# Performance work log

Hardware: AMD Instinct MI355X
Metric: run time of the kernel (lower is better)

The kernel has to match this reference:

```python
import jax, jax.numpy as jnp
import numpy as np
from jax import lax

D_MODEL = 1024
D_STATE = 16
D_CONV = 4
EXPAND = 2
D_INNER = D_MODEL * EXPAND
EPS = 1e-6


def setup_inputs() -> dict:
    key = jax.random.key(0)
    ks = jax.random.split(key, 8)
    B, L = 2, 1024
    x = jax.random.normal(ks[0], (B, L, D_MODEL), dtype=jnp.float32)
    norm_w = jnp.ones((D_MODEL,), jnp.float32)
    W_in = jax.random.normal(ks[1], (2 * D_INNER, D_MODEL), jnp.float32) * (1.0 / np.sqrt(D_MODEL))
    conv_w = jax.random.normal(ks[2], (D_INNER, 1, D_CONV), jnp.float32) * (1.0 / np.sqrt(D_CONV))
    conv_b = jnp.zeros((D_INNER,), jnp.float32)
    W_x = jax.random.normal(ks[3], (2 * D_STATE + 1, D_INNER), jnp.float32) * (1.0 / np.sqrt(D_INNER))
    A_log = jnp.log(jnp.broadcast_to(jnp.arange(1, D_STATE + 1, dtype=jnp.float32), (D_INNER, D_STATE)))
    D_skip = jnp.ones((D_INNER,), jnp.float32)
    W_dt = jax.random.normal(ks[4], (D_INNER, 1), jnp.float32)
    b_dt = jax.random.normal(ks[5], (D_INNER,), jnp.float32) * 0.1
    W_out = jax.random.normal(ks[6], (D_MODEL, D_INNER), jnp.float32) * (1.0 / np.sqrt(D_INNER))
    return {"x": x, "norm_w": norm_w, "W_in": W_in, "conv_w": conv_w, "conv_b": conv_b,
            "W_x": W_x, "A_log": A_log, "D_skip": D_skip, "W_dt": W_dt, "b_dt": b_dt, "W_out": W_out}


def _selective_scan(x, delta, A, Bp, Cp, D_skip):
    # x, delta: (B, L, D); A: (D, N); Bp, Cp: (B, L, N)
    Bb, L, Dd = x.shape
    N = A.shape[1]

    def step(h, t_in):
        delta_t, B_t, C_t, x_t = t_in           # (B,D),(B,N),(B,N),(B,D)
        dA = jnp.exp(delta_t[..., None] * A)    # (B,D,N)
        h = dA * h + (delta_t * x_t)[..., None] * B_t[:, None, :]
        y_t = jnp.einsum('bdn,bn->bd', h, C_t)
        return h, y_t

    xs = (jnp.moveaxis(delta, 1, 0), jnp.moveaxis(Bp, 1, 0),
          jnp.moveaxis(Cp, 1, 0), jnp.moveaxis(x, 1, 0))
    h0 = jnp.zeros((Bb, Dd, N), x.dtype)
    _, ys = lax.scan(step, h0, xs)              # ys: (L,B,D)
    return jnp.moveaxis(ys, 0, 1) + x * D_skip


def reference(x, norm_w, W_in, conv_w, conv_b, W_x, A_log, D_skip, W_dt, b_dt, W_out):
    residual = x
    # RMSNorm
    xn = x * lax.rsqrt(jnp.mean(x * x, axis=-1, keepdims=True) + EPS) * norm_w
    # in_proj and split
    xz = xn @ W_in.T                              # (B,L,2*Din)
    x_ssm, z = jnp.split(xz, 2, axis=-1)
    # causal depthwise conv1d
    xc = jnp.swapaxes(x_ssm, 1, 2)                # (B,Din,L)
    xc = lax.conv_general_dilated(xc, conv_w, window_strides=(1,),
                                  padding=[(D_CONV - 1, 0)],
                                  feature_group_count=D_INNER,
                                  dimension_numbers=('NCH', 'OIH', 'NCH'))
    xc = xc + conv_b[None, :, None]
    x_ssm = jax.nn.silu(jnp.swapaxes(xc, 1, 2))   # (B,L,Din)
    # input-dependent SSM params
    ssm_params = x_ssm @ W_x.T                    # (B,L,2N+1)
    B_param = ssm_params[:, :, :D_STATE]
    C_param = ssm_params[:, :, D_STATE:2 * D_STATE]
    dt_raw = ssm_params[:, :, -1:]                # (B,L,1)
    delta = jax.nn.softplus(dt_raw * W_dt[:, 0] + b_dt)  # (B,L,Din)
    A = -jnp.exp(A_log)
    y = _selective_scan(x_ssm, delta, A, B_param, C_param, D_skip)
    y = y * jax.nn.silu(z)
    y = y @ W_out.T
    return y + residual
```

## Files before the change

kernel.cpp:

```cpp
#include <hip/hip_runtime.h>
#include <math.h>

#define D_MODEL 1024
#define D_STATE 16
#define D_CONV  4
#define D_INNER 2048
#define LSEQ    1024
#define BATCH   2
#define NROWS   (BATCH * LSEQ)
#define EPSV    1e-6f

#define CHUNK   32
#define NCHUNK  (LSEQ / CHUNK)
#define SSTATE  (BATCH * D_INNER * D_STATE)
#define SROW    36

typedef __attribute__((ext_vector_type(8))) short bf16x8;
typedef __attribute__((ext_vector_type(4))) float f32x4;

__device__ __forceinline__ float silu_f(float x) { return x / (1.0f + __expf(-x)); }
__device__ __forceinline__ float softplus_f(float x) {
    return (x > 20.0f) ? x : __logf(1.0f + __expf(x));
}
__device__ __forceinline__ unsigned short f2bf(float f) {
    unsigned int u = __float_as_uint(f);
    unsigned int r = (u + 0x7FFFu + ((u >> 16) & 1u)) >> 16;
    return (unsigned short)r;
}

#define WIN_F4   (2 * D_INNER * D_MODEL / 4)
#define WOUT_F4  (D_MODEL * D_INNER / 4)
__global__ __launch_bounds__(256) void cvt_both_kernel(const float* __restrict__ w_in,
                                                       unsigned short* __restrict__ w_in_b,
                                                       const float* __restrict__ w_out,
                                                       unsigned short* __restrict__ w_out_b) {
    int i = blockIdx.x * 256 + threadIdx.x;
    const float* src;
    unsigned short* dst;
    int j;
    if (i < WIN_F4) { src = w_in;  dst = w_in_b;  j = i; }
    else            { src = w_out; dst = w_out_b; j = i - WIN_F4; }
    float4 v = ((const float4*)src)[j];
    ushort4 o;
    o.x = f2bf(v.x); o.y = f2bf(v.y); o.z = f2bf(v.z); o.w = f2bf(v.w);
    ((ushort4*)dst)[j] = o;
}

__global__ __launch_bounds__(256) void rmsnorm_kernel(const float* __restrict__ x,
                                                      const float* __restrict__ w,
                                                      unsigned short* __restrict__ xnb) {
    int row = blockIdx.x;
    const float4* xr = (const float4*)(x + (size_t)row * D_MODEL);
    float4 v = xr[threadIdx.x];
    float s = v.x * v.x + v.y * v.y + v.z * v.z + v.w * v.w;
#pragma unroll
    for (int off = 32; off > 0; off >>= 1) s += __shfl_down(s, off, 64);
    __shared__ float wsum[4];
    int lane = threadIdx.x & 63, wv = threadIdx.x >> 6;
    if (lane == 0) wsum[wv] = s;
    __syncthreads();
    float tot = wsum[0] + wsum[1] + wsum[2] + wsum[3];
    float scale = rsqrtf(tot * (1.0f / D_MODEL) + EPSV);
    const float4* wr = (const float4*)w;
    float4 wv4 = wr[threadIdx.x];
    ushort4 o;
    o.x = f2bf(v.x * scale * wv4.x);
    o.y = f2bf(v.y * scale * wv4.y);
    o.z = f2bf(v.z * scale * wv4.z);
    o.w = f2bf(v.w * scale * wv4.w);
    ((ushort4*)(xnb + (size_t)row * D_MODEL))[threadIdx.x] = o;
}

template<int TM, int TN, int JL>
__global__ __launch_bounds__(256) void gemm_bt_db(const short* __restrict__ A,
                                                  const short* __restrict__ B,
                                                  float* __restrict__ C,
                                                  const float* __restrict__ resid,
                                                  int M, int N, int Klen, int ld) {
    constexpr int MI = TM / 32, NJ = TN / 32;
    __shared__ alignas(16) short As[2][TM * 32];
    __shared__ alignas(16) short Bs[2][TN * 32];
    int tid = threadIdx.x;
    int wave = tid >> 6, lane = tid & 63;
    int wm = (wave >> 1) * (TM / 2), wn = (wave & 1) * (TN / 2);
    int m0 = blockIdx.y * TM, n0 = blockIdx.x * TN;
    int koff = blockIdx.z * Klen;
    C += (size_t)blockIdx.z * M * N;

    f32x4 acc[MI][NJ];
#pragma unroll
    for (int i = 0; i < MI; i++)
#pragma unroll
        for (int j = 0; j < NJ; j++) acc[i][j] = (f32x4){0.f, 0.f, 0.f, 0.f};

    const short* Ab = A + (size_t)m0 * ld + koff;
    const short* Bb = B + (size_t)n0 * ld + koff;
    int qk = (lane >> 4) * 8;
    int rr = lane & 15;

    auto stage = [&](int k0, int buf) {
#pragma unroll
        for (int c0 = 0; c0 < TM * 4; c0 += 256) {
            int c = c0 + tid;
            __builtin_amdgcn_global_load_lds(
                (const __attribute__((address_space(1))) void*)(Ab + (size_t)(c >> 2) * ld + k0 + (c & 3) * 8),
                (__attribute__((address_space(3))) void*)(&As[buf][c * 8]), 16, 0, 0);
        }
#pragma unroll
        for (int c0 = 0; c0 < TN * 4; c0 += 256) {
            int c = c0 + tid;
            __builtin_amdgcn_global_load_lds(
                (const __attribute__((address_space(1))) void*)(Bb + (size_t)(c >> 2) * ld + k0 + (c & 3) * 8),
                (__attribute__((address_space(3))) void*)(&Bs[buf][c * 8]), 16, 0, 0);
        }
    };

    stage(0, 0);
    int KI = Klen / 32;
    for (int ki = 0; ki < KI; ki++) {
        int b = ki & 1;
        if (ki + 1 < KI) {
            stage((ki + 1) * 32, b ^ 1);
            __builtin_amdgcn_s_waitcnt(0xF70 | JL);
        } else {
            __builtin_amdgcn_s_waitcnt(0xF70);
        }
        __builtin_amdgcn_s_barrier();

        bf16x8 af[MI], bfr[NJ];
#pragma unroll
        for (int i = 0; i < MI; i++)
            af[i] = *(const bf16x8*)(&As[b][(wm + i * 16 + rr) * 32 + qk]);
#pragma unroll
        for (int j = 0; j < NJ; j++)
            bfr[j] = *(const bf16x8*)(&Bs[b][(wn + j * 16 + rr) * 32 + qk]);
#pragma unroll
        for (int i = 0; i < MI; i++)
#pragma unroll
            for (int j = 0; j < NJ; j++)
                acc[i][j] = __builtin_amdgcn_mfma_f32_16x16x32_bf16(af[i], bfr[j], acc[i][j], 0, 0, 0);
        __builtin_amdgcn_s_barrier();
    }

    int q4 = (lane >> 4) * 4;
#pragma unroll
    for (int i = 0; i < MI; i++) {
#pragma unroll
        for (int j = 0; j < NJ; j++) {
            int n = n0 + wn + j * 16 + rr;
#pragma unroll
            for (int v = 0; v < 4; v++) {
                int mm = m0 + wm + i * 16 + q4 + v;
                float val = acc[i][j][v];
                if (resid) val += resid[(size_t)mm * N + n];
                C[(size_t)mm * N + n] = val;
            }
        }
    }
}

__global__ __launch_bounds__(256) void splitk_reduce_kernel(const float* __restrict__ p,
                                                            const float* __restrict__ resid,
                                                            float* __restrict__ out) {
    int i = blockIdx.x * 256 + threadIdx.x;
    float4 a = ((const float4*)p)[i];
    float4 b = ((const float4*)(p + (size_t)NROWS * D_MODEL))[i];
    float4 r = ((const float4*)resid)[i];
    float4 o;
    o.x = a.x + b.x + r.x; o.y = a.y + b.y + r.y;
    o.z = a.z + b.z + r.z; o.w = a.w + b.w + r.w;
    ((float4*)out)[i] = o;
}

__global__ __launch_bounds__(256) void conv_silu_kernel(const float* __restrict__ xz,
                                                        const float* __restrict__ w,
                                                        const float* __restrict__ cb,
                                                        float* __restrict__ xc) {
    int idx = blockIdx.x * 256 + threadIdx.x;
    int d = idx & (D_INNER - 1);
    int bl = idx >> 11;
    int l = bl & (LSEQ - 1);
    int bb = bl >> 10;
    float w0 = w[d * 4 + 0], w1 = w[d * 4 + 1], w2 = w[d * 4 + 2], w3 = w[d * 4 + 3];
    const float* base = xz + (size_t)(bb * LSEQ) * (2 * D_INNER) + d;
    float acc = cb[d];
    if (l >= 3) acc += w0 * base[(size_t)(l - 3) * (2 * D_INNER)];
    if (l >= 2) acc += w1 * base[(size_t)(l - 2) * (2 * D_INNER)];
    if (l >= 1) acc += w2 * base[(size_t)(l - 1) * (2 * D_INNER)];
    acc += w3 * base[(size_t)l * (2 * D_INNER)];
    xc[idx] = silu_f(acc);
}

#define PR 4
__global__ __launch_bounds__(256) void params_kernel(const float* __restrict__ xc,
                                                     const float* __restrict__ Wx,
                                                     float* __restrict__ ssm) {
    int r0 = blockIdx.x * PR;
    __shared__ alignas(16) float xs[PR][D_INNER];
    const float4* src = (const float4*)(xc + (size_t)r0 * D_INNER);
    for (int i = threadIdx.x; i < PR * D_INNER / 4; i += 256)
        ((float4*)xs)[i] = src[i];
    __syncthreads();
    int lane = threadIdx.x & 63, wv = threadIdx.x >> 6;
    for (int n = wv; n < 2 * D_STATE + 1; n += 4) {
        const float4* wrow = (const float4*)(Wx + (size_t)n * D_INNER);
        float s0 = 0.f, s1 = 0.f, s2 = 0.f, s3 = 0.f;
#pragma unroll
        for (int c = 0; c < D_INNER / 4 / 64; c++) {
            int k = c * 64 + lane;
            float4 w  = wrow[k];
            float4 a0 = *(const float4*)&xs[0][k * 4];
            float4 a1 = *(const float4*)&xs[1][k * 4];
            float4 a2 = *(const float4*)&xs[2][k * 4];
            float4 a3 = *(const float4*)&xs[3][k * 4];
            s0 += a0.x * w.x + a0.y * w.y + a0.z * w.z + a0.w * w.w;
            s1 += a1.x * w.x + a1.y * w.y + a1.z * w.z + a1.w * w.w;
            s2 += a2.x * w.x + a2.y * w.y + a2.z * w.z + a2.w * w.w;
            s3 += a3.x * w.x + a3.y * w.y + a3.z * w.z + a3.w * w.w;
        }
#pragma unroll
        for (int off = 32; off > 0; off >>= 1) {
            s0 += __shfl_down(s0, off, 64);
            s1 += __shfl_down(s1, off, 64);
            s2 += __shfl_down(s2, off, 64);
            s3 += __shfl_down(s3, off, 64);
        }
        if (lane == 0) {
            ssm[(size_t)(r0 + 0) * 33 + n] = s0;
            ssm[(size_t)(r0 + 1) * 33 + n] = s1;
            ssm[(size_t)(r0 + 2) * 33 + n] = s2;
            ssm[(size_t)(r0 + 3) * 33 + n] = s3;
        }
    }
}


__device__ __forceinline__ void stage_ssm(const float* __restrict__ ssm,
                                          float* __restrict__ s_ssm,
                                          int bb, int c, int tid) {
    int t = tid >> 3, j = tid & 7;
    const float* g = ssm + (size_t)(bb * LSEQ + c * CHUNK + t) * 33;
    float* s = s_ssm + t * SROW;
    for (int col = j; col < 33; col += 8) s[col] = g[col];
}

__global__ __launch_bounds__(256) void scanA_kernel(const float* __restrict__ ssm,
                                                    const float* __restrict__ xc,
                                                    const float* __restrict__ Wdt,
                                                    const float* __restrict__ bdt,
                                                    float* __restrict__ P,
                                                    float* __restrict__ Q) {
    int c = blockIdx.x, dg = blockIdx.y, bb = blockIdx.z;
    int tid = threadIdx.x;
    int d = dg * 256 + tid;
    __shared__ alignas(16) float s_ssm[CHUNK * SROW];
    stage_ssm(ssm, s_ssm, bb, c, tid);
    __syncthreads();

    float wdt = Wdt[d], bdtv = bdt[d];
    float h[16];
#pragma unroll
    for (int n = 0; n < 16; n++) h[n] = 0.f;
    float sd = 0.f;
    const float* xg = xc + ((size_t)(bb * LSEQ + c * CHUNK)) * D_INNER + d;

#pragma unroll 2
    for (int t = 0; t < CHUNK; t++) {
        float dtr = s_ssm[t * SROW + 32];
        float dlt = softplus_f(dtr * wdt + bdtv);
        float xt = xg[(size_t)t * D_INNER];
        float u = dlt * xt;
        sd += dlt;
        float e1 = __expf(-dlt);
        float ek = 1.f;
        const float4* Bq = (const float4*)&s_ssm[t * SROW];
#pragma unroll
        for (int r = 0; r < 4; r++) {
            float4 Bv = Bq[r];
            ek *= e1; h[r * 4 + 0] = ek * h[r * 4 + 0] + u * Bv.x;
            ek *= e1; h[r * 4 + 1] = ek * h[r * 4 + 1] + u * Bv.y;
            ek *= e1; h[r * 4 + 2] = ek * h[r * 4 + 2] + u * Bv.z;
            ek *= e1; h[r * 4 + 3] = ek * h[r * 4 + 3] + u * Bv.w;
        }
    }
    size_t idx = (size_t)c * SSTATE + ((size_t)bb * D_INNER + d) * 16;
    float E = __expf(-sd);
    float pk = 1.f;
#pragma unroll
    for (int r = 0; r < 4; r++) {
        float4 pv, qv;
        pk *= E; pv.x = pk;
        pk *= E; pv.y = pk;
        pk *= E; pv.z = pk;
        pk *= E; pv.w = pk;
        qv.x = h[r * 4 + 0]; qv.y = h[r * 4 + 1];
        qv.z = h[r * 4 + 2]; qv.w = h[r * 4 + 3];
        *(float4*)(P + idx + r * 4) = pv;
        *(float4*)(Q + idx + r * 4) = qv;
    }
}

__global__ __launch_bounds__(256) void scanB_kernel(float* __restrict__ P,
                                                    const float* __restrict__ Q) {
    int bdn = blockIdx.x * 256 + threadIdx.x;
    float H = 0.0f;
#pragma unroll
    for (int c = 0; c < NCHUNK; c++) {
        size_t idx = (size_t)c * SSTATE + bdn;
        float p = P[idx], q = Q[idx];
        P[idx] = H;
        H = p * H + q;
    }
}

__global__ __launch_bounds__(256) void scanC_kernel(const float* __restrict__ ssm,
                                                    const float* __restrict__ xc,
                                                    const float* __restrict__ xz,
                                                    const float* __restrict__ Wdt,
                                                    const float* __restrict__ bdt,
                                                    const float* __restrict__ Hs,
                                                    const float* __restrict__ Dskip,
                                                    unsigned short* __restrict__ yb) {
    int c = blockIdx.x, dg = blockIdx.y, bb = blockIdx.z;
    int tid = threadIdx.x;
    int d = dg * 256 + tid;
    __shared__ alignas(16) float s_ssm[CHUNK * SROW];
    stage_ssm(ssm, s_ssm, bb, c, tid);
    __syncthreads();

    float wdt = Wdt[d], bdtv = bdt[d], dsk = Dskip[d];
    float h[16];
    {
        size_t idx = (size_t)c * SSTATE + ((size_t)bb * D_INNER + d) * 16;
#pragma unroll
        for (int r = 0; r < 4; r++) {
            float4 hv = *(const float4*)(Hs + idx + r * 4);
            h[r * 4 + 0] = hv.x; h[r * 4 + 1] = hv.y;
            h[r * 4 + 2] = hv.z; h[r * 4 + 3] = hv.w;
        }
    }
    const float* xg = xc + ((size_t)(bb * LSEQ + c * CHUNK)) * D_INNER + d;
    const float* zg = xz + ((size_t)(bb * LSEQ + c * CHUNK)) * (2 * D_INNER) + D_INNER + d;
    unsigned short* yg = yb + ((size_t)(bb * LSEQ + c * CHUNK)) * D_INNER + d;

#pragma unroll 2
    for (int t = 0; t < CHUNK; t++) {
        float dtr = s_ssm[t * SROW + 32];
        float dlt = softplus_f(dtr * wdt + bdtv);
        float xt = xg[(size_t)t * D_INNER];
        float zt = zg[(size_t)t * (2 * D_INNER)];
        float u = dlt * xt;
        float e1 = __expf(-dlt);
        float ek = 1.f;
        const float4* Bq = (const float4*)&s_ssm[t * SROW];
        const float4* Cq = (const float4*)&s_ssm[t * SROW + 16];
        float y = 0.f;
#pragma unroll
        for (int r = 0; r < 4; r++) {
            float4 Bv = Bq[r];
            float4 Cv = Cq[r];
            ek *= e1; h[r * 4 + 0] = ek * h[r * 4 + 0] + u * Bv.x;
            ek *= e1; h[r * 4 + 1] = ek * h[r * 4 + 1] + u * Bv.y;
            ek *= e1; h[r * 4 + 2] = ek * h[r * 4 + 2] + u * Bv.z;
            ek *= e1; h[r * 4 + 3] = ek * h[r * 4 + 3] + u * Bv.w;
            y += h[r * 4 + 0] * Cv.x + h[r * 4 + 1] * Cv.y
               + h[r * 4 + 2] * Cv.z + h[r * 4 + 3] * Cv.w;
        }
        float o = (y + xt * dsk) * silu_f(zt);
        yg[(size_t)t * D_INNER] = f2bf(o);
    }
}

extern "C" void kernel_launch(void* const* d_in, const int* in_sizes, int n_in,
                              void* d_out, int out_size, void* d_ws, size_t ws_size,
                              hipStream_t stream) {
    const float* x      = (const float*)d_in[0];
    const float* norm_w = (const float*)d_in[1];
    const float* W_in   = (const float*)d_in[2];
    const float* conv_w = (const float*)d_in[3];
    const float* conv_b = (const float*)d_in[4];
    const float* W_x    = (const float*)d_in[5];
    const float* D_skip = (const float*)d_in[7];
    const float* W_dt   = (const float*)d_in[8];
    const float* b_dt   = (const float*)d_in[9];
    const float* W_out  = (const float*)d_in[10];
    float* out = (float*)d_out;

    float* ws = (float*)d_ws;
    float* xz      = ws;
    float* xconv   = xz + (size_t)NROWS * 2 * D_INNER;
    float* ssm     = xconv + (size_t)NROWS * D_INNER;
    float* after   = ssm + (size_t)NROWS * 33;
    unsigned short* xnb    = (unsigned short*)after;
    unsigned short* W_in_b = (unsigned short*)(after + 1024 * 1024);
    unsigned short* W_out_b= (unsigned short*)(after + 3 * 1024 * 1024);
    unsigned short* ybuf_b = (unsigned short*)(after + 4 * 1024 * 1024);
    float* Pbuf  = after;
    float* Qbuf  = after + 4 * 1024 * 1024;
    float* Cpart = after + 6 * 1024 * 1024;

    cvt_both_kernel<<<(WIN_F4 + WOUT_F4) / 256, 256, 0, stream>>>(W_in, W_in_b, W_out, W_out_b);
    rmsnorm_kernel<<<NROWS, 256, 0, stream>>>(x, norm_w, xnb);
    {
        dim3 grid(2 * D_INNER / 128, NROWS / 128, 1);
        gemm_bt_db<128, 128, 4><<<grid, 256, 0, stream>>>(
            (const short*)xnb, (const short*)W_in_b, xz, nullptr,
            NROWS, 2 * D_INNER, D_MODEL, D_MODEL);
    }
    conv_silu_kernel<<<(NROWS * D_INNER) / 256, 256, 0, stream>>>(xz, conv_w, conv_b, xconv);
    params_kernel<<<NROWS / PR, 256, 0, stream>>>(xconv, W_x, ssm);
    {
        dim3 grid(NCHUNK, D_INNER / 256, BATCH);
        scanA_kernel<<<grid, 256, 0, stream>>>(ssm, xconv, W_dt, b_dt, Pbuf, Qbuf);
        scanB_kernel<<<SSTATE / 256, 256, 0, stream>>>(Pbuf, Qbuf);
        scanC_kernel<<<grid, 256, 0, stream>>>(ssm, xconv, xz, W_dt, b_dt,
                                               Pbuf, D_skip, ybuf_b);
    }
    {
        dim3 grid(D_MODEL / 64, NROWS / 64, 2);
        gemm_bt_db<64, 64, 2><<<grid, 256, 0, stream>>>(
            (const short*)ybuf_b, (const short*)W_out_b, Cpart, nullptr,
            NROWS, D_MODEL, D_INNER / 2, D_INNER);
        splitk_reduce_kernel<<<(NROWS * D_MODEL) / 1024, 256, 0, stream>>>(Cpart, x, out);
    }
}
```

Before: 224.9 us.

## Store in_proj output as bf16 and fuse conv+SiLU into SSM params kernel

The in_proj GEMM now writes its xz output in bf16 rather than fp32, which halves the bytes written and later read by the conv and scanC kernels. The separate conv_silu kernel is folded into the params kernel: each block computes the causal conv and SiLU for its rows into shared memory, also writes xconv to global, then does the W_x projection. This removes one launch and one fp32 re-read of xconv. The cost is lower precision for x_ssm and z, and strided 2-byte loads from bf16 rows in the conv.

```diff
diff --git a/kernel.cpp b/kernel.cpp
--- a/kernel.cpp
+++ b/kernel.cpp
@@ -26,6 +26,9 @@
     unsigned int u = __float_as_uint(f);
     unsigned int r = (u + 0x7FFFu + ((u >> 16) & 1u)) >> 16;
     return (unsigned short)r;
+}
+__device__ __forceinline__ float bf2f(unsigned short s) {
+    return __uint_as_float((unsigned int)s << 16);
 }
 
 #define WIN_F4   (2 * D_INNER * D_MODEL / 4)
@@ -71,10 +74,10 @@
     ((ushort4*)(xnb + (size_t)row * D_MODEL))[threadIdx.x] = o;
 }
 
-template<int TM, int TN, int JL>
+template<int TM, int TN, int JL, bool BF16OUT>
 __global__ __launch_bounds__(256) void gemm_bt_db(const short* __restrict__ A,
                                                   const short* __restrict__ B,
-                                                  float* __restrict__ C,
+                                                  void* __restrict__ Cv,
                                                   const float* __restrict__ resid,
                                                   int M, int N, int Klen, int ld) {
     constexpr int MI = TM / 32, NJ = TN / 32;
@@ -85,7 +88,7 @@
     int wm = (wave >> 1) * (TM / 2), wn = (wave & 1) * (TN / 2);
     int m0 = blockIdx.y * TM, n0 = blockIdx.x * TN;
     int koff = blockIdx.z * Klen;
-    C += (size_t)blockIdx.z * M * N;
+    size_t zoff = (size_t)blockIdx.z * M * N;
 
     f32x4 acc[MI][NJ];
 #pragma unroll
@@ -153,7 +156,9 @@
                 int mm = m0 + wm + i * 16 + q4 + v;
                 float val = acc[i][j][v];
                 if (resid) val += resid[(size_t)mm * N + n];
-                C[(size_t)mm * N + n] = val;
+                size_t off = (size_t)mm * N + n + zoff;
+                if constexpr (BF16OUT) ((unsigned short*)Cv)[off] = f2bf(val);
+                else                   ((float*)Cv)[off] = val;
             }
         }
     }
@@ -172,51 +177,52 @@
     ((float4*)out)[i] = o;
 }
 
-__global__ __launch_bounds__(256) void conv_silu_kernel(const float* __restrict__ xz,
-                                                        const float* __restrict__ w,
-                                                        const float* __restrict__ cb,
-                                                        float* __restrict__ xc) {
-    int idx = blockIdx.x * 256 + threadIdx.x;
-    int d = idx & (D_INNER - 1);
-    int bl = idx >> 11;
-    int l = bl & (LSEQ - 1);
-    int bb = bl >> 10;
-    float w0 = w[d * 4 + 0], w1 = w[d * 4 + 1], w2 = w[d * 4 + 2], w3 = w[d * 4 + 3];
-    const float* base = xz + (size_t)(bb * LSEQ) * (2 * D_INNER) + d;
-    float acc = cb[d];
-    if (l >= 3) acc += w0 * base[(size_t)(l - 3) * (2 * D_INNER)];
-    if (l >= 2) acc += w1 * base[(size_t)(l - 2) * (2 * D_INNER)];
-    if (l >= 1) acc += w2 * base[(size_t)(l - 1) * (2 * D_INNER)];
-    acc += w3 * base[(size_t)l * (2 * D_INNER)];
-    xc[idx] = silu_f(acc);
-}
-
 #define PR 4
-__global__ __launch_bounds__(256) void params_kernel(const float* __restrict__ xc,
-                                                     const float* __restrict__ Wx,
-                                                     float* __restrict__ ssm) {
+__global__ __launch_bounds__(256) void conv_params_kernel(const unsigned short* __restrict__ xzb,
+                                                          const float* __restrict__ w,
+                                                          const float* __restrict__ cb,
+                                                          const float* __restrict__ Wx,
+                                                          float* __restrict__ xconv,
+                                                          float* __restrict__ ssm) {
     int r0 = blockIdx.x * PR;
+    int tid = threadIdx.x;
     __shared__ alignas(16) float xs[PR][D_INNER];
-    const float4* src = (const float4*)(xc + (size_t)r0 * D_INNER);
-    for (int i = threadIdx.x; i < PR * D_INNER / 4; i += 256)
-        ((float4*)xs)[i] = src[i];
+
+#pragma unroll
+    for (int i = 0; i < PR * D_INNER / 256; i++) {
+        int f = i * 256 + tid;
+        int row = f >> 11;
+        int d = f & (D_INNER - 1);
+        int gr = r0 + row;
+        int l = gr & (LSEQ - 1);
+        const unsigned short* p = xzb + (size_t)gr * (2 * D_INNER) + d;
+        float w0 = w[d * 4 + 0], w1 = w[d * 4 + 1], w2 = w[d * 4 + 2], w3 = w[d * 4 + 3];
+        float acc = cb[d] + w3 * bf2f(p[0]);
+        if (l >= 1) acc += w2 * bf2f(p[-1 * (2 * D_INNER)]);
+        if (l >= 2) acc += w1 * bf2f(p[-2 * (2 * D_INNER)]);
+        if (l >= 3) acc += w0 * bf2f(p[-3 * (2 * D_INNER)]);
+        float v = silu_f(acc);
+        xs[row][d] = v;
+        xconv[(size_t)gr * D_INNER + d] = v;
+    }
     __syncthreads();
-    int lane = threadIdx.x & 63, wv = threadIdx.x >> 6;
+
+    int lane = tid & 63, wv = tid >> 6;
     for (int n = wv; n < 2 * D_STATE + 1; n += 4) {
         const float4* wrow = (const float4*)(Wx + (size_t)n * D_INNER);
         float s0 = 0.f, s1 = 0.f, s2 = 0.f, s3 = 0.f;
 #pragma unroll
         for (int c = 0; c < D_INNER / 4 / 64; c++) {
             int k = c * 64 + lane;
-            float4 w  = wrow[k];
+            float4 wt = wrow[k];
             float4 a0 = *(const float4*)&xs[0][k * 4];
             float4 a1 = *(const float4*)&xs[1][k * 4];
             float4 a2 = *(const float4*)&xs[2][k * 4];
             float4 a3 = *(const float4*)&xs[3][k * 4];
-            s0 += a0.x * w.x + a0.y * w.y + a0.z * w.z + a0.w * w.w;
-            s1 += a1.x * w.x + a1.y * w.y + a1.z * w.z + a1.w * w.w;
-            s2 += a2.x * w.x + a2.y * w.y + a2.z * w.z + a2.w * w.w;
-            s3 += a3.x * w.x + a3.y * w.y + a3.z * w.z + a3.w * w.w;
+            s0 += a0.x * wt.x + a0.y * wt.y + a0.z * wt.z + a0.w * wt.w;
+            s1 += a1.x * wt.x + a1.y * wt.y + a1.z * wt.z + a1.w * wt.w;
+            s2 += a2.x * wt.x + a2.y * wt.y + a2.z * wt.z + a2.w * wt.w;
+            s3 += a3.x * wt.x + a3.y * wt.y + a3.z * wt.z + a3.w * wt.w;
         }
 #pragma unroll
         for (int off = 32; off > 0; off >>= 1) {
@@ -315,7 +321,7 @@
 
 __global__ __launch_bounds__(256) void scanC_kernel(const float* __restrict__ ssm,
                                                     const float* __restrict__ xc,
-                                                    const float* __restrict__ xz,
+                                                    const unsigned short* __restrict__ xzb,
                                                     const float* __restrict__ Wdt,
                                                     const float* __restrict__ bdt,
                                                     const float* __restrict__ Hs,
@@ -340,7 +346,7 @@
         }
     }
     const float* xg = xc + ((size_t)(bb * LSEQ + c * CHUNK)) * D_INNER + d;
-    const float* zg = xz + ((size_t)(bb * LSEQ + c * CHUNK)) * (2 * D_INNER) + D_INNER + d;
+    const unsigned short* zg = xzb + ((size_t)(bb * LSEQ + c * CHUNK)) * (2 * D_INNER) + D_INNER + d;
     unsigned short* yg = yb + ((size_t)(bb * LSEQ + c * CHUNK)) * D_INNER + d;
 
 #pragma unroll 2
@@ -348,7 +354,7 @@
         float dtr = s_ssm[t * SROW + 32];
         float dlt = softplus_f(dtr * wdt + bdtv);
         float xt = xg[(size_t)t * D_INNER];
-        float zt = zg[(size_t)t * (2 * D_INNER)];
+        float zt = bf2f(zg[(size_t)t * (2 * D_INNER)]);
         float u = dlt * xt;
         float e1 = __expf(-dlt);
         float ek = 1.f;
@@ -387,8 +393,8 @@
     float* out = (float*)d_out;
 
     float* ws = (float*)d_ws;
-    float* xz      = ws;
-    float* xconv   = xz + (size_t)NROWS * 2 * D_INNER;
+    unsigned short* xzb = (unsigned short*)ws;
+    float* xconv   = ws + 4 * 1024 * 1024;
     float* ssm     = xconv + (size_t)NROWS * D_INNER;
     float* after   = ssm + (size_t)NROWS * 33;
     unsigned short* xnb    = (unsigned short*)after;
@@ -403,22 +409,22 @@
     rmsnorm_kernel<<<NROWS, 256, 0, stream>>>(x, norm_w, xnb);
     {
         dim3 grid(2 * D_INNER / 128, NROWS / 128, 1);
-        gemm_bt_db<128, 128, 4><<<grid, 256, 0, stream>>>(
-            (const short*)xnb, (const short*)W_in_b, xz, nullptr,
+        gemm_bt_db<128, 128, 4, true><<<grid, 256, 0, stream>>>(
+            (const short*)xnb, (const short*)W_in_b, xzb, nullptr,
             NROWS, 2 * D_INNER, D_MODEL, D_MODEL);
     }
-    conv_silu_kernel<<<(NROWS * D_INNER) / 256, 256, 0, stream>>>(xz, conv_w, conv_b, xconv);
-    params_kernel<<<NROWS / PR, 256, 0, stream>>>(xconv, W_x, ssm);
+    conv_params_kernel<<<NROWS / PR, 256, 0, stream>>>(xzb, conv_w, conv_b, W_x,
+                                                       xconv, ssm);
     {
         dim3 grid(NCHUNK, D_INNER / 256, BATCH);
         scanA_kernel<<<grid, 256, 0, stream>>>(ssm, xconv, W_dt, b_dt, Pbuf, Qbuf);
         scanB_kernel<<<SSTATE / 256, 256, 0, stream>>>(Pbuf, Qbuf);
-        scanC_kernel<<<grid, 256, 0, stream>>>(ssm, xconv, xz, W_dt, b_dt,
+        scanC_kernel<<<grid, 256, 0, stream>>>(ssm, xconv, xzb, W_dt, b_dt,
                                                Pbuf, D_skip, ybuf_b);
     }
     {
         dim3 grid(D_MODEL / 64, NROWS / 64, 2);
-        gemm_bt_db<64, 64, 2><<<grid, 256, 0, stream>>>(
+        gemm_bt_db<64, 64, 2, false><<<grid, 256, 0, stream>>>(
             (const short*)ybuf_b, (const short*)W_out_b, Cpart, nullptr,
             NROWS, D_MODEL, D_INNER / 2, D_INNER);
         splitk_reduce_kernel<<<(NROWS * D_MODEL) / 1024, 256, 0, stream>>>(Cpart, x, out);
```

After: 232.1 us. 3.2% more time.
